# Optimization experiments

Hardware: AMD Instinct MI355X
Metric: run time of the kernel (lower is better)

The kernel has to match this reference:

```python
import jax, jax.numpy as jnp
import numpy as np

B, H, SQ, SKV, D, TOPK = 1, 16, 1024, 4096, 128, 64


def setup_inputs() -> dict:
    key = jax.random.key(0)
    kq, kk, kv, ki, ks = jax.random.split(key, 5)
    q = jax.random.normal(kq, (B, H, SQ, D), dtype=jnp.float32)
    k = jax.random.normal(kk, (B, H, SKV, D), dtype=jnp.float32)
    v = jax.random.normal(kv, (B, H, SKV, D), dtype=jnp.float32)
    topk_indices = jax.random.randint(ki, (B, SQ, TOPK), 0, SKV, dtype=jnp.int32)
    topk_scores = jax.random.uniform(ks, (B, SQ, TOPK), dtype=jnp.float32)
    return {"q": q, "k": k, "v": v, "topk_indices": topk_indices,
            "topk_scores": topk_scores}


def reference(q, k, v, topk_indices, topk_scores):
    # q: (b,h,s,d); k,v: (b,h,S,d) global (cp_world_size=1 all-gather is identity)
    head_dim = q.shape[-1]
    scale = head_dim ** -0.5
    # Gather selected K/V per query without dense (b,h,s,S,d) expansion.
    # idx: (b,1,s,topk,1) broadcast against (b,h,1,S,d) along axis=3.
    idx = topk_indices[:, None, :, :, None]
    k_g = jnp.take_along_axis(k[:, :, None, :, :], idx, axis=3)  # (b,h,s,t,d)
    v_g = jnp.take_along_axis(v[:, :, None, :, :], idx, axis=3)  # (b,h,s,t,d)
    scores = jnp.einsum("bhsd,bhstd->bhst", q, k_g) * scale
    w = jax.nn.softmax(scores, axis=-1)
    # rescale by indexer scores and renormalize
    w = w * topk_scores[:, None, :, :]
    w = w / (jnp.sum(w, axis=-1, keepdims=True) + 1e-12)
    out = jnp.einsum("bhst,bhstd->bhsd", w, v_g)
    return out
```

## Files before the change

### kernel.cpp

```cpp
#include <hip/hip_runtime.h>

#define NH  16
#define SQL 1024
#define SKV 4096
#define HD  128
#define TK  64

__global__ __launch_bounds__(256) void dsa_sparse_attn(
    const float* __restrict__ q, const float* __restrict__ k,
    const float* __restrict__ v, const int* __restrict__ tidx,
    const float* __restrict__ tsc, float* __restrict__ out)
{
    __shared__ int   idxs[4][TK];
    __shared__ float wsc[4][TK];

    const int tid  = threadIdx.x;
    const int wv   = tid >> 6;
    const int lane = tid & 63;
    const int half = lane >> 5;
    const int l32  = lane & 31;
    const int bi   = blockIdx.x;

    const int h = ((bi & 7) << 1) | ((bi >> 3) & 1);
    const int s = ((bi >> 4) << 2) + wv;

    const float* qp = q + (size_t)(h * SQL + s) * HD;
    const float4 qf = *(const float4*)(qp + 4 * l32);

    const int   t_idx = tidx[s * TK + lane];
    const float t_sc  = tsc[s * TK + lane];
    idxs[wv][lane] = t_idx;
    (void)t_idx;

    const float* kb = k + (size_t)h * SKV * HD;
#pragma unroll 4
    for (int i = 0; i < TK / 2; ++i) {
        const int t   = 2 * i + half;
        const int row = idxs[wv][t];
        float4 k4 = *(const float4*)(kb + (size_t)row * HD + 4 * l32);
        float d = k4.x * qf.x + k4.y * qf.y + k4.z * qf.z + k4.w * qf.w;
        d += __shfl_xor(d, 16);
        d += __shfl_xor(d, 8);
        d += __shfl_xor(d, 4);
        d += __shfl_xor(d, 2);
        d += __shfl_xor(d, 1);
        if (l32 == 0) wsc[wv][t] = d;
    }

    float acc = wsc[wv][lane] * 0.08838834764831845f;
    float m = acc;
#pragma unroll
    for (int off = 32; off; off >>= 1) m = fmaxf(m, __shfl_xor(m, off));
    const float e   = __expf(acc - m);
    const float ets = e * t_sc;
    float se = e, sets = ets;
#pragma unroll
    for (int off = 32; off; off >>= 1) {
        se   += __shfl_xor(se, off);
        sets += __shfl_xor(sets, off);
    }
    wsc[wv][lane] = ets / (sets + 1e-12f * se);

    const float* vb = v + (size_t)h * SKV * HD;
    float4 o = make_float4(0.f, 0.f, 0.f, 0.f);
#pragma unroll 4
    for (int i = 0; i < TK / 2; ++i) {
        const int t    = 2 * i + half;
        const int row  = idxs[wv][t];
        const float wt = wsc[wv][t];
        float4 v4 = *(const float4*)(vb + (size_t)row * HD + 4 * l32);
        o.x += wt * v4.x;
        o.y += wt * v4.y;
        o.z += wt * v4.z;
        o.w += wt * v4.w;
    }
    o.x += __shfl_xor(o.x, 32);
    o.y += __shfl_xor(o.y, 32);
    o.z += __shfl_xor(o.z, 32);
    o.w += __shfl_xor(o.w, 32);

    if (half == 0) {
        *(float4*)(out + (size_t)(h * SQL + s) * HD + 4 * l32) = o;
    }
}

extern "C" void kernel_launch(void* const* d_in, const int* in_sizes, int n_in,
                              void* d_out, int out_size, void* d_ws, size_t ws_size,
                              hipStream_t stream) {
    const float* q  = (const float*)d_in[0];
    const float* k  = (const float*)d_in[1];
    const float* v  = (const float*)d_in[2];
    const int*   ti = (const int*)d_in[3];
    const float* ts = (const float*)d_in[4];
    float* out = (float*)d_out;

    dsa_sparse_attn<<<dim3(4096), dim3(256), 0, stream>>>(q, k, v, ti, ts, out);
}
```

Before: 165.3 us.

## Split fused sparse attention into separate QK-softmax and PV kernels

The fused kernel becomes two launches. The first computes the gathered QK scores, softmax and topk rescale, and writes the normalized weights to workspace. The second gathers V rows and applies those weights. The block-to-(head, query) mapping also changes so that 8 heads share a cache working set at a time. The intent is to keep only K (then only V) resident in cache per phase, which should improve L2/MALL hit rates for the random row gathers. The cost is an extra launch, a round trip of the weights through global memory, and in the fallback path an in-place stash inside the output buffer.

```diff
diff --git a/kernel.cpp b/kernel.cpp
--- a/kernel.cpp
+++ b/kernel.cpp
@@ -6,10 +6,15 @@
 #define HD  128
 #define TK  64
 
-__global__ __launch_bounds__(256) void dsa_sparse_attn(
+__device__ __forceinline__ void map_hs(int bi, int wv, int& h, int& s) {
+    h = ((bi >> 11) << 3) | (bi & 7);
+    s = (((bi >> 3) & 255) << 2) + wv;
+}
+
+__global__ __launch_bounds__(256) void qk_softmax_k(
     const float* __restrict__ q, const float* __restrict__ k,
-    const float* __restrict__ v, const int* __restrict__ tidx,
-    const float* __restrict__ tsc, float* __restrict__ out)
+    const int* __restrict__ tidx, const float* __restrict__ tsc,
+    float* __restrict__ wstash)
 {
     __shared__ int   idxs[4][TK];
     __shared__ float wsc[4][TK];
@@ -19,18 +24,14 @@
     const int lane = tid & 63;
     const int half = lane >> 5;
     const int l32  = lane & 31;
-    const int bi   = blockIdx.x;
-
-    const int h = ((bi & 7) << 1) | ((bi >> 3) & 1);
-    const int s = ((bi >> 4) << 2) + wv;
+    int h, s;
+    map_hs(blockIdx.x, wv, h, s);
 
     const float* qp = q + (size_t)(h * SQL + s) * HD;
     const float4 qf = *(const float4*)(qp + 4 * l32);
 
-    const int   t_idx = tidx[s * TK + lane];
-    const float t_sc  = tsc[s * TK + lane];
-    idxs[wv][lane] = t_idx;
-    (void)t_idx;
+    const float t_sc = tsc[s * TK + lane];
+    idxs[wv][lane] = tidx[s * TK + lane];
 
     const float* kb = k + (size_t)h * SKV * HD;
 #pragma unroll 4
@@ -59,7 +60,29 @@
         se   += __shfl_xor(se, off);
         sets += __shfl_xor(sets, off);
     }
-    wsc[wv][lane] = ets / (sets + 1e-12f * se);
+    wstash[(size_t)(h * SQL + s) * TK + lane] = ets / (sets + 1e-12f * se);
+}
+
+template <int STASH_IN_OUT>
+__global__ __launch_bounds__(256) void pv_k(
+    const float* __restrict__ v, const int* __restrict__ tidx,
+    const float* __restrict__ wstash, float* __restrict__ out)
+{
+    __shared__ int   idxs[4][TK];
+    __shared__ float wgts[4][TK];
+
+    const int tid  = threadIdx.x;
+    const int wv   = tid >> 6;
+    const int lane = tid & 63;
+    const int half = lane >> 5;
+    const int l32  = lane & 31;
+    int h, s;
+    map_hs(blockIdx.x, wv, h, s);
+
+    const size_t hs = (size_t)(h * SQL + s);
+    idxs[wv][lane] = tidx[s * TK + lane];
+    wgts[wv][lane] = STASH_IN_OUT ? wstash[hs * HD + lane]
+                                  : wstash[hs * TK + lane];
 
     const float* vb = v + (size_t)h * SKV * HD;
     float4 o = make_float4(0.f, 0.f, 0.f, 0.f);
@@ -67,7 +90,7 @@
     for (int i = 0; i < TK / 2; ++i) {
         const int t    = 2 * i + half;
         const int row  = idxs[wv][t];
-        const float wt = wsc[wv][t];
+        const float wt = wgts[wv][t];
         float4 v4 = *(const float4*)(vb + (size_t)row * HD + 4 * l32);
         o.x += wt * v4.x;
         o.y += wt * v4.y;
@@ -80,7 +103,7 @@
     o.w += __shfl_xor(o.w, 32);
 
     if (half == 0) {
-        *(float4*)(out + (size_t)(h * SQL + s) * HD + 4 * l32) = o;
+        *(float4*)(out + hs * HD + 4 * l32) = o;
     }
 }
 
@@ -94,5 +117,13 @@
     const float* ts = (const float*)d_in[4];
     float* out = (float*)d_out;
 
-    dsa_sparse_attn<<<dim3(4096), dim3(256), 0, stream>>>(q, k, v, ti, ts, out);
+    const size_t need = (size_t)NH * SQL * TK * sizeof(float);
+    if (ws_size >= need) {
+        float* ws = (float*)d_ws;
+        qk_softmax_k<<<dim3(4096), dim3(256), 0, stream>>>(q, k, ti, ts, ws);
+        pv_k<0><<<dim3(4096), dim3(256), 0, stream>>>(v, ti, ws, out);
+    } else {
+        qk_softmax_k<<<dim3(4096), dim3(256), 0, stream>>>(q, k, ti, ts, out);
+        pv_k<1><<<dim3(4096), dim3(256), 0, stream>>>(v, ti, out, out);
+    }
 }
```

Result: faster. 161.4 us (-2.4%).

## Convert K/V to bf16 in workspace before sparse attention gather

Applied to the files above, without the earlier changes.

Adds a pre-pass that converts the full K and V tensors to bf16 in the workspace, then runs the gather-attention kernel on the bf16 copies with 16 lanes per row. It also remaps blocks to heads differently. The aim is to halve the bytes moved by the random row gathers. In exchange, each call must read all of K and V once (64 MB of fp32) and write 32 MB of bf16, which is far more than the gathered footprint. It also lowers precision, and it keeps an fp32 fallback for when the workspace is too small.

```diff
diff --git a/kernel.cpp b/kernel.cpp
--- a/kernel.cpp
+++ b/kernel.cpp
@@ -6,9 +6,34 @@
 #define HD  128
 #define TK  64
 
-__global__ __launch_bounds__(256) void dsa_sparse_attn(
-    const float* __restrict__ q, const float* __restrict__ k,
-    const float* __restrict__ v, const int* __restrict__ tidx,
+__device__ __forceinline__ float blo(unsigned u) { return __uint_as_float(u << 16); }
+__device__ __forceinline__ float bhi(unsigned u) { return __uint_as_float(u & 0xFFFF0000u); }
+
+__global__ __launch_bounds__(256) void cvt_bf16(const float* __restrict__ src,
+                                                unsigned short* __restrict__ dst,
+                                                int n8) {
+    int i = blockIdx.x * 256 + threadIdx.x;
+    if (i >= n8) return;
+    const float4* s4 = (const float4*)src;
+    float4 a = s4[2 * i], b = s4[2 * i + 1];
+    float f[8] = {a.x, a.y, a.z, a.w, b.x, b.y, b.z, b.w};
+    unsigned r[8];
+#pragma unroll
+    for (int j = 0; j < 8; ++j) {
+        unsigned u = __float_as_uint(f[j]);
+        r[j] = (u + 0x7FFFu + ((u >> 16) & 1u)) >> 16;
+    }
+    uint4 o;
+    o.x = r[0] | (r[1] << 16);
+    o.y = r[2] | (r[3] << 16);
+    o.z = r[4] | (r[5] << 16);
+    o.w = r[6] | (r[7] << 16);
+    ((uint4*)dst)[i] = o;
+}
+
+__global__ __launch_bounds__(256) void dsa_bf16(
+    const float* __restrict__ q, const unsigned short* __restrict__ kb16,
+    const unsigned short* __restrict__ vb16, const int* __restrict__ tidx,
     const float* __restrict__ tsc, float* __restrict__ out)
 {
     __shared__ int   idxs[4][TK];
@@ -17,34 +42,36 @@
     const int tid  = threadIdx.x;
     const int wv   = tid >> 6;
     const int lane = tid & 63;
-    const int half = lane >> 5;
-    const int l32  = lane & 31;
+    const int quad = lane >> 4;
+    const int l16  = lane & 15;
     const int bi   = blockIdx.x;
 
-    const int h = ((bi & 7) << 1) | ((bi >> 3) & 1);
-    const int s = ((bi >> 4) << 2) + wv;
+    const int h = ((bi >> 11) << 3) | (bi & 7);
+    const int s = (((bi >> 3) & 255) << 2) + wv;
 
-    const float* qp = q + (size_t)(h * SQL + s) * HD;
-    const float4 qf = *(const float4*)(qp + 4 * l32);
+    const float* qp = q + (size_t)(h * SQL + s) * HD + 8 * l16;
+    const float4 qa = *(const float4*)qp;
+    const float4 qb = *(const float4*)(qp + 4);
 
-    const int   t_idx = tidx[s * TK + lane];
-    const float t_sc  = tsc[s * TK + lane];
-    idxs[wv][lane] = t_idx;
-    (void)t_idx;
+    idxs[wv][lane] = tidx[s * TK + lane];
+    const float t_sc = tsc[s * TK + lane];
 
-    const float* kb = k + (size_t)h * SKV * HD;
-#pragma unroll 4
-    for (int i = 0; i < TK / 2; ++i) {
-        const int t   = 2 * i + half;
+    const unsigned short* kb = kb16 + (size_t)h * SKV * HD;
+#pragma unroll 8
+    for (int i = 0; i < TK / 4; ++i) {
+        const int t   = 4 * i + quad;
         const int row = idxs[wv][t];
-        float4 k4 = *(const float4*)(kb + (size_t)row * HD + 4 * l32);
-        float d = k4.x * qf.x + k4.y * qf.y + k4.z * qf.z + k4.w * qf.w;
-        d += __shfl_xor(d, 16);
+        uint4 kw = *(const uint4*)(kb + (size_t)row * HD + 8 * l16);
+        float d;
+        d  = qa.x * blo(kw.x) + qa.y * bhi(kw.x);
+        d += qa.z * blo(kw.y) + qa.w * bhi(kw.y);
+        d += qb.x * blo(kw.z) + qb.y * bhi(kw.z);
+        d += qb.z * blo(kw.w) + qb.w * bhi(kw.w);
         d += __shfl_xor(d, 8);
         d += __shfl_xor(d, 4);
         d += __shfl_xor(d, 2);
         d += __shfl_xor(d, 1);
-        if (l32 == 0) wsc[wv][t] = d;
+        if (l16 == 0) wsc[wv][t] = d;
     }
 
     float acc = wsc[wv][lane] * 0.08838834764831845f;
@@ -61,27 +88,77 @@
     }
     wsc[wv][lane] = ets / (sets + 1e-12f * se);
 
-    const float* vb = v + (size_t)h * SKV * HD;
+    const unsigned short* vb = vb16 + (size_t)h * SKV * HD;
+    float o[8] = {0.f, 0.f, 0.f, 0.f, 0.f, 0.f, 0.f, 0.f};
+#pragma unroll 8
+    for (int i = 0; i < TK / 4; ++i) {
+        const int t    = 4 * i + quad;
+        const int row  = idxs[wv][t];
+        const float wt = wsc[wv][t];
+        uint4 vw = *(const uint4*)(vb + (size_t)row * HD + 8 * l16);
+        o[0] += wt * blo(vw.x);  o[1] += wt * bhi(vw.x);
+        o[2] += wt * blo(vw.y);  o[3] += wt * bhi(vw.y);
+        o[4] += wt * blo(vw.z);  o[5] += wt * bhi(vw.z);
+        o[6] += wt * blo(vw.w);  o[7] += wt * bhi(vw.w);
+    }
+#pragma unroll
+    for (int j = 0; j < 8; ++j) {
+        o[j] += __shfl_xor(o[j], 16);
+        o[j] += __shfl_xor(o[j], 32);
+    }
+    if (quad == 0) {
+        float* op = out + (size_t)(h * SQL + s) * HD + 8 * l16;
+        *(float4*)op       = make_float4(o[0], o[1], o[2], o[3]);
+        *(float4*)(op + 4) = make_float4(o[4], o[5], o[6], o[7]);
+    }
+}
+
+__global__ __launch_bounds__(256) void dsa_fp32(
+    const float* __restrict__ q, const float* __restrict__ k,
+    const float* __restrict__ v, const int* __restrict__ tidx,
+    const float* __restrict__ tsc, float* __restrict__ out)
+{
+    __shared__ int   idxs[4][TK];
+    __shared__ float wsc[4][TK];
+    const int tid = threadIdx.x, wv = tid >> 6, lane = tid & 63;
+    const int half = lane >> 5, l32 = lane & 31, bi = blockIdx.x;
+    const int h = ((bi & 7) << 1) | ((bi >> 3) & 1);
+    const int s = ((bi >> 4) << 2) + wv;
+    const float* qp = q + (size_t)(h * SQL + s) * HD;
+    const float4 qf = *(const float4*)(qp + 4 * l32);
+    const float t_sc = tsc[s * TK + lane];
+    idxs[wv][lane] = tidx[s * TK + lane];
+    const float* kb = k + (size_t)h * SKV * HD;
+#pragma unroll 4
+    for (int i = 0; i < TK / 2; ++i) {
+        const int t = 2 * i + half, row = idxs[wv][t];
+        float4 k4 = *(const float4*)(kb + (size_t)row * HD + 4 * l32);
+        float d = k4.x * qf.x + k4.y * qf.y + k4.z * qf.z + k4.w * qf.w;
+        d += __shfl_xor(d, 16); d += __shfl_xor(d, 8); d += __shfl_xor(d, 4);
+        d += __shfl_xor(d, 2);  d += __shfl_xor(d, 1);
+        if (l32 == 0) wsc[wv][t] = d;
+    }
+    float acc = wsc[wv][lane] * 0.08838834764831845f;
+    float m = acc;
+#pragma unroll
+    for (int off = 32; off; off >>= 1) m = fmaxf(m, __shfl_xor(m, off));
+    const float e = __expf(acc - m), ets = e * t_sc;
+    float se = e, sets = ets;
+#pragma unroll
+    for (int off = 32; off; off >>= 1) { se += __shfl_xor(se, off); sets += __shfl_xor(sets, off); }
+    wsc[wv][lane] = ets / (sets + 1e-12f * se);
+    const float* vbp = v + (size_t)h * SKV * HD;
     float4 o = make_float4(0.f, 0.f, 0.f, 0.f);
 #pragma unroll 4
     for (int i = 0; i < TK / 2; ++i) {
-        const int t    = 2 * i + half;
-        const int row  = idxs[wv][t];
+        const int t = 2 * i + half, row = idxs[wv][t];
         const float wt = wsc[wv][t];
-        float4 v4 = *(const float4*)(vb + (size_t)row * HD + 4 * l32);
-        o.x += wt * v4.x;
-        o.y += wt * v4.y;
-        o.z += wt * v4.z;
-        o.w += wt * v4.w;
+        float4 v4 = *(const float4*)(vbp + (size_t)row * HD + 4 * l32);
+        o.x += wt * v4.x; o.y += wt * v4.y; o.z += wt * v4.z; o.w += wt * v4.w;
     }
-    o.x += __shfl_xor(o.x, 32);
-    o.y += __shfl_xor(o.y, 32);
-    o.z += __shfl_xor(o.z, 32);
-    o.w += __shfl_xor(o.w, 32);
-
-    if (half == 0) {
-        *(float4*)(out + (size_t)(h * SQL + s) * HD + 4 * l32) = o;
-    }
+    o.x += __shfl_xor(o.x, 32); o.y += __shfl_xor(o.y, 32);
+    o.z += __shfl_xor(o.z, 32); o.w += __shfl_xor(o.w, 32);
+    if (half == 0) *(float4*)(out + (size_t)(h * SQL + s) * HD + 4 * l32) = o;
 }
 
 extern "C" void kernel_launch(void* const* d_in, const int* in_sizes, int n_in,
@@ -94,5 +171,16 @@
     const float* ts = (const float*)d_in[4];
     float* out = (float*)d_out;
 
-    dsa_sparse_attn<<<dim3(4096), dim3(256), 0, stream>>>(q, k, v, ti, ts, out);
+    const size_t nkv  = (size_t)NH * SKV * HD;
+    const size_t need = 2 * nkv * sizeof(unsigned short);
+    if (ws_size >= need) {
+        unsigned short* kb16 = (unsigned short*)d_ws;
+        unsigned short* vb16 = kb16 + nkv;
+        const int n8 = (int)(nkv / 8);
+        cvt_bf16<<<dim3(n8 / 256), dim3(256), 0, stream>>>(k, kb16, n8);
+        cvt_bf16<<<dim3(n8 / 256), dim3(256), 0, stream>>>(v, vb16, n8);
+        dsa_bf16<<<dim3(4096), dim3(256), 0, stream>>>(q, kb16, vb16, ti, ts, out);
+    } else {
+        dsa_fp32<<<dim3(4096), dim3(256), 0, stream>>>(q, k, v, ti, ts, out);
+    }
 }
```

After: 144.4 us. -12.6%, faster.
